# Kernel tuning notes

Hardware: AMD Instinct MI355X
Metric: run time of the kernel (lower is better)

Reference implementation:

```python
import jax, jax.numpy as jnp
import numpy as np

L, D, N = 4096, 1024, 16  # seq_len, d_model, hiddens_per_input


def setup_inputs() -> dict:
    key = jax.random.key(0)
    ks = jax.random.split(key, 9)
    x = jax.random.normal(ks[0], (L, D), dtype=jnp.float32)
    # Delta param (pre-softplus); softplus(Delta) > 0 is the discretization step
    Delta = jax.random.normal(ks[1], (D,), dtype=jnp.float32)
    # A stored as (re, im); default scheme uses A_re = -1 (stable), theta in [0, 2pi)
    A_re = -(0.5 + 0.5 * jax.random.uniform(ks[2], (D, N), dtype=jnp.float32))
    A_im = jax.random.uniform(ks[3], (D, N), dtype=jnp.float32) * 2.0 * jnp.pi
    scale = 1.0 / jnp.sqrt(jnp.float32(D))  # matrix_init: randn / sqrt(shape[0])
    B_re = jax.random.normal(ks[4], (D, N), dtype=jnp.float32) * scale
    B_im = jax.random.normal(ks[5], (D, N), dtype=jnp.float32) * scale
    C_re = jax.random.normal(ks[6], (D, N), dtype=jnp.float32) * scale
    C_im = jax.random.normal(ks[7], (D, N), dtype=jnp.float32) * scale
    D_param = jax.random.normal(ks[8], (D,), dtype=jnp.float32) * scale
    return {"x": x, "Delta": Delta, "A_re": A_re, "A_im": A_im,
            "B_re": B_re, "B_im": B_im, "C_re": C_re, "C_im": C_im,
            "D_param": D_param}


def _binary_operator_diag(q_i, q_j):
    """Associative op for diagonal linear recurrence h_j = A_j h_{j-1} + b_j."""
    A_i, b_i = q_i
    A_j, b_j = q_j
    return (A_j * A_i, A_j * b_i + b_j)


def reference(x, Delta, A_re, A_im, B_re, B_im, C_re, C_im, D_param):
    Bc = B_re + 1j * B_im                      # (D, N) complex
    Cc = C_re + 1j * C_im                      # (D, N) complex
    Ac = A_re + 1j * A_im                      # (D, N) complex
    dt = jax.nn.softplus(Delta)                # (D,)
    # shared_Delta=True branch: Lambda = exp(dt[:, None] * A), repeated over L
    Lam = jnp.exp(dt[:, None] * Ac)            # (D, N) complex
    Lambda_elements = jnp.broadcast_to(Lam[None, :, :], (x.shape[0], *Lam.shape))
    # Bu = einsum('D, D N, L D -> L D N', dt, B, x)
    Bu_elements = jnp.einsum('D,DN,LD->LDN', dt.astype(Bc.dtype), Bc,
                             x.astype(Bc.dtype))
    _, hidden_states = jax.lax.associative_scan(
        _binary_operator_diag, (Lambda_elements, Bu_elements))  # (L, D, N)
    out = jnp.einsum('LDN,DN->LD', hidden_states, Cc) + D_param[None, :] * x
    return out.real
```

## Files before the change

### kernel.cpp

```cpp
#include <hip/hip_runtime.h>
#include <math.h>

constexpr int L   = 4096;
constexpr int D   = 1024;
constexpr int N   = 16;
constexpr int CPB = 2;
constexpr int NB  = D / CPB;
constexpr int NCB = 64;
constexpr int T   = L / NCB;

__device__ __forceinline__ float softplus_f(float v) {
    return fmaxf(v, 0.0f) + log1pf(expf(-fabsf(v)));
}

__device__ __forceinline__ void lam_fast(float ar, float ai, float dt,
                                         float& lr, float& li) {
    float e = __expf(ar * dt);
    float s, c;
    __sincosf(ai * dt, &s, &c);
    lr = e * c;
    li = e * s;
}

__global__ __launch_bounds__(256, 2) void k_fused(
    const float* __restrict__ x,
    const float* __restrict__ Delta,
    const float* __restrict__ A_re, const float* __restrict__ A_im,
    const float* __restrict__ B_re, const float* __restrict__ B_im,
    const float* __restrict__ C_re, const float* __restrict__ C_im,
    const float* __restrict__ Dp,
    float* __restrict__ out)
{
    __shared__ float  xs[T * 128];
    __shared__ float2 sums[NCB * 32];

    const int b  = blockIdx.x;
    const int d0 = (b & 7) * 128 + (b >> 3) * 2;
    const int t  = threadIdx.x;

    {
        const int sct = t & 63;
        const int si  = t >> 6;
        float2 v[16];
        #pragma unroll
        for (int k = 0; k < 16; ++k) {
            int l = sct * T + si * 16 + k;
            v[k] = *(const float2*)(x + (size_t)l * D + d0);
        }
        #pragma unroll
        for (int k = 0; k < 16; ++k) {
            int i = si * 16 + k;
            *(float2*)&xs[i * 128 + sct * 2] = v[k];
        }
    }

    const int h  = t & 1;
    const int dd = (t >> 1) & 1;
    const int ct = t >> 2;
    const int d  = d0 + dd;
    const float dt = softplus_f(Delta[d]);

    float Lr[8], Li[8];
    {
        const int base = d * N + h * 8;
        float4 a0 = *(const float4*)(A_re + base);
        float4 a1 = *(const float4*)(A_re + base + 4);
        float4 m0 = *(const float4*)(A_im + base);
        float4 m1 = *(const float4*)(A_im + base + 4);
        const float ar[8] = {a0.x, a0.y, a0.z, a0.w, a1.x, a1.y, a1.z, a1.w};
        const float ai[8] = {m0.x, m0.y, m0.z, m0.w, m1.x, m1.y, m1.z, m1.w};
        #pragma unroll
        for (int j = 0; j < 8; ++j) lam_fast(ar[j], ai[j], dt, Lr[j], Li[j]);
    }
    __syncthreads();

    float gr[8] = {0, 0, 0, 0, 0, 0, 0, 0}, gi[8] = {0, 0, 0, 0, 0, 0, 0, 0};
    #pragma unroll 8
    for (int i = 0; i < T; ++i) {
        float xv = xs[i * 128 + ct * 2 + dd];
        #pragma unroll
        for (int j = 0; j < 8; ++j) {
            float t2 = fmaf(-Li[j], gi[j], xv);
            float nr = fmaf(Lr[j], gr[j], t2);
            gi[j] = fmaf(Lr[j], gi[j], Li[j] * gr[j]);
            gr[j] = nr;
        }
    }
    {
        float2* sp = &sums[ct * 32 + dd * 16 + h * 8];
        #pragma unroll
        for (int j = 0; j < 8; ++j) sp[j] = make_float2(gr[j], gi[j]);
    }
    __syncthreads();

    if (t < 32) {
        const int dd2 = t >> 4, n2 = t & 15;
        const int d2  = d0 + dd2;
        const float dt2 = softplus_f(Delta[d2]);
        float lr, li;
        lam_fast(A_re[d2 * N + n2], A_im[d2 * N + n2], dt2, lr, li);
        #pragma unroll
        for (int k = 0; k < 6; ++k) {
            float nr = lr * lr - li * li;
            li = 2.0f * lr * li;
            lr = nr;
        }
        float cr = 0.0f, ci = 0.0f;
        #pragma unroll
        for (int c0 = 0; c0 < NCB; c0 += 16) {
            float2 sv[16];
            #pragma unroll
            for (int u = 0; u < 16; ++u) sv[u] = sums[(c0 + u) * 32 + t];
            #pragma unroll
            for (int u = 0; u < 16; ++u) {
                sums[(c0 + u) * 32 + t] = make_float2(cr, ci);
                float nr = fmaf(lr, cr, fmaf(-li, ci, sv[u].x));
                ci = fmaf(lr, ci, fmaf(li, cr, sv[u].y));
                cr = nr;
            }
        }
    }

    float Cr[8], Ci[8];
    {
        const int base = d * N + h * 8;
        float4 b0 = *(const float4*)(B_re + base);
        float4 b1 = *(const float4*)(B_re + base + 4);
        float4 e0 = *(const float4*)(B_im + base);
        float4 e1 = *(const float4*)(B_im + base + 4);
        float4 f0 = *(const float4*)(C_re + base);
        float4 f1 = *(const float4*)(C_re + base + 4);
        float4 g0 = *(const float4*)(C_im + base);
        float4 g1 = *(const float4*)(C_im + base + 4);
        const float br[8] = {b0.x, b0.y, b0.z, b0.w, b1.x, b1.y, b1.z, b1.w};
        const float bi[8] = {e0.x, e0.y, e0.z, e0.w, e1.x, e1.y, e1.z, e1.w};
        const float cr[8] = {f0.x, f0.y, f0.z, f0.w, f1.x, f1.y, f1.z, f1.w};
        const float ci[8] = {g0.x, g0.y, g0.z, g0.w, g1.x, g1.y, g1.z, g1.w};
        #pragma unroll
        for (int j = 0; j < 8; ++j) {
            Cr[j] = dt * (cr[j] * br[j] - ci[j] * bi[j]);
            Ci[j] = dt * (cr[j] * bi[j] + ci[j] * br[j]);
        }
    }
    const float dpv = Dp[d];
    __syncthreads();

    {
        const float2* cp = &sums[ct * 32 + dd * 16 + h * 8];
        #pragma unroll
        for (int j = 0; j < 8; ++j) { gr[j] = cp[j].x; gi[j] = cp[j].y; }
    }
    #pragma unroll 4
    for (int ib = 0; ib < T / 2; ++ib) {
        float keep = 0.0f;
        #pragma unroll
        for (int u = 0; u < 2; ++u) {
            int i = ib * 2 + u;
            float xv = xs[i * 128 + ct * 2 + dd];
            float acc = 0.0f;
            #pragma unroll
            for (int j = 0; j < 8; ++j) {
                float t2 = fmaf(-Li[j], gi[j], xv);
                float nr = fmaf(Lr[j], gr[j], t2);
                gi[j] = fmaf(Lr[j], gi[j], Li[j] * gr[j]);
                gr[j] = nr;
                acc = fmaf(Cr[j], gr[j], acc);
                acc = fmaf(-Ci[j], gi[j], acc);
            }
            acc += __shfl_xor(acc, 1);
            acc = fmaf(dpv, xv, acc);
            keep = (h == u) ? acc : keep;
        }
        out[(size_t)(ct * T + ib * 2 + h) * D + d] = keep;
    }
}

extern "C" void kernel_launch(void* const* d_in, const int* in_sizes, int n_in,
                              void* d_out, int out_size, void* d_ws, size_t ws_size,
                              hipStream_t stream) {
    const float* x     = (const float*)d_in[0];
    const float* Delta = (const float*)d_in[1];
    const float* A_re  = (const float*)d_in[2];
    const float* A_im  = (const float*)d_in[3];
    const float* B_re  = (const float*)d_in[4];
    const float* B_im  = (const float*)d_in[5];
    const float* C_re  = (const float*)d_in[6];
    const float* C_im  = (const float*)d_in[7];
    const float* Dp    = (const float*)d_in[8];
    float* out = (float*)d_out;

    k_fused<<<NB, 256, 0, stream>>>(x, Delta, A_re, A_im, B_re, B_im,
                                    C_re, C_im, Dp, out);
}
```

Baseline: 106.9 us.

## Double chunk count to 128 with 512 threads and pack recurrence into float2 FMAs

```diff
diff --git a/kernel.cpp b/kernel.cpp
--- a/kernel.cpp
+++ b/kernel.cpp
@@ -6,8 +6,11 @@
 constexpr int N   = 16;
 constexpr int CPB = 2;
 constexpr int NB  = D / CPB;
-constexpr int NCB = 64;
+constexpr int NCB = 128;
 constexpr int T   = L / NCB;
+constexpr int NT  = 512;
+
+typedef float v2 __attribute__((ext_vector_type(2)));
 
 __device__ __forceinline__ float softplus_f(float v) {
     return fmaxf(v, 0.0f) + log1pf(expf(-fabsf(v)));
@@ -22,7 +25,11 @@
     li = e * s;
 }
 
-__global__ __launch_bounds__(256, 2) void k_fused(
+__device__ __forceinline__ v2 vfma(v2 a, v2 b, v2 c) {
+    return __builtin_elementwise_fma(a, b, c);
+}
+
+__global__ __launch_bounds__(NT, 4) void k_fused(
     const float* __restrict__ x,
     const float* __restrict__ Delta,
     const float* __restrict__ A_re, const float* __restrict__ A_im,
@@ -31,7 +38,7 @@
     const float* __restrict__ Dp,
     float* __restrict__ out)
 {
-    __shared__ float  xs[T * 128];
+    __shared__ float  xs[T * 256];
     __shared__ float2 sums[NCB * 32];
 
     const int b  = blockIdx.x;
@@ -39,18 +46,18 @@
     const int t  = threadIdx.x;
 
     {
-        const int sct = t & 63;
-        const int si  = t >> 6;
-        float2 v[16];
-        #pragma unroll
-        for (int k = 0; k < 16; ++k) {
-            int l = sct * T + si * 16 + k;
+        const int sct = t & 127;
+        const int si  = t >> 7;
+        float2 v[8];
+        #pragma unroll
+        for (int k = 0; k < 8; ++k) {
+            int l = sct * T + si * 8 + k;
             v[k] = *(const float2*)(x + (size_t)l * D + d0);
         }
         #pragma unroll
-        for (int k = 0; k < 16; ++k) {
-            int i = si * 16 + k;
-            *(float2*)&xs[i * 128 + sct * 2] = v[k];
+        for (int k = 0; k < 8; ++k) {
+            int il = si * 8 + k;
+            *(float2*)&xs[il * 256 + sct * 2] = v[k];
         }
     }
 
@@ -60,7 +67,7 @@
     const int d  = d0 + dd;
     const float dt = softplus_f(Delta[d]);
 
-    float Lr[8], Li[8];
+    v2 LR[4], LI[4];
     {
         const int base = d * N + h * 8;
         float4 a0 = *(const float4*)(A_re + base);
@@ -70,26 +77,37 @@
         const float ar[8] = {a0.x, a0.y, a0.z, a0.w, a1.x, a1.y, a1.z, a1.w};
         const float ai[8] = {m0.x, m0.y, m0.z, m0.w, m1.x, m1.y, m1.z, m1.w};
         #pragma unroll
-        for (int j = 0; j < 8; ++j) lam_fast(ar[j], ai[j], dt, Lr[j], Li[j]);
+        for (int p = 0; p < 4; ++p) {
+            float lr0, li0, lr1, li1;
+            lam_fast(ar[2 * p], ai[2 * p], dt, lr0, li0);
+            lam_fast(ar[2 * p + 1], ai[2 * p + 1], dt, lr1, li1);
+            LR[p] = (v2){lr0, lr1};
+            LI[p] = (v2){li0, li1};
+        }
     }
     __syncthreads();
 
-    float gr[8] = {0, 0, 0, 0, 0, 0, 0, 0}, gi[8] = {0, 0, 0, 0, 0, 0, 0, 0};
-    #pragma unroll 8
+    v2 GR[4] = {(v2)0, (v2)0, (v2)0, (v2)0};
+    v2 GI[4] = {(v2)0, (v2)0, (v2)0, (v2)0};
+    #pragma unroll 4
     for (int i = 0; i < T; ++i) {
-        float xv = xs[i * 128 + ct * 2 + dd];
-        #pragma unroll
-        for (int j = 0; j < 8; ++j) {
-            float t2 = fmaf(-Li[j], gi[j], xv);
-            float nr = fmaf(Lr[j], gr[j], t2);
-            gi[j] = fmaf(Lr[j], gi[j], Li[j] * gr[j]);
-            gr[j] = nr;
+        float xv = xs[i * 256 + ct * 2 + dd];
+        v2 XV = (v2){xv, xv};
+        #pragma unroll
+        for (int p = 0; p < 4; ++p) {
+            v2 t2 = vfma(-LI[p], GI[p], XV);
+            v2 nr = vfma(LR[p], GR[p], t2);
+            GI[p] = vfma(LR[p], GI[p], LI[p] * GR[p]);
+            GR[p] = nr;
         }
     }
     {
         float2* sp = &sums[ct * 32 + dd * 16 + h * 8];
         #pragma unroll
-        for (int j = 0; j < 8; ++j) sp[j] = make_float2(gr[j], gi[j]);
+        for (int p = 0; p < 4; ++p) {
+            sp[2 * p]     = make_float2(GR[p].x, GI[p].x);
+            sp[2 * p + 1] = make_float2(GR[p].y, GI[p].y);
+        }
     }
     __syncthreads();
 
@@ -100,7 +118,7 @@
         float lr, li;
         lam_fast(A_re[d2 * N + n2], A_im[d2 * N + n2], dt2, lr, li);
         #pragma unroll
-        for (int k = 0; k < 6; ++k) {
+        for (int k = 0; k < 5; ++k) {
             float nr = lr * lr - li * li;
             li = 2.0f * lr * li;
             lr = nr;
@@ -121,7 +139,7 @@
         }
     }
 
-    float Cr[8], Ci[8];
+    v2 CR[4], CI[4];
     {
         const int base = d * N + h * 8;
         float4 b0 = *(const float4*)(B_re + base);
@@ -137,9 +155,11 @@
         const float cr[8] = {f0.x, f0.y, f0.z, f0.w, f1.x, f1.y, f1.z, f1.w};
         const float ci[8] = {g0.x, g0.y, g0.z, g0.w, g1.x, g1.y, g1.z, g1.w};
         #pragma unroll
-        for (int j = 0; j < 8; ++j) {
-            Cr[j] = dt * (cr[j] * br[j] - ci[j] * bi[j]);
-            Ci[j] = dt * (cr[j] * bi[j] + ci[j] * br[j]);
+        for (int p = 0; p < 4; ++p) {
+            CR[p] = (v2){dt * (cr[2*p] * br[2*p] - ci[2*p] * bi[2*p]),
+                         dt * (cr[2*p+1] * br[2*p+1] - ci[2*p+1] * bi[2*p+1])};
+            CI[p] = (v2){dt * (cr[2*p] * bi[2*p] + ci[2*p] * br[2*p]),
+                         dt * (cr[2*p+1] * bi[2*p+1] + ci[2*p+1] * br[2*p+1])};
         }
     }
     const float dpv = Dp[d];
@@ -148,7 +168,11 @@
     {
         const float2* cp = &sums[ct * 32 + dd * 16 + h * 8];
         #pragma unroll
-        for (int j = 0; j < 8; ++j) { gr[j] = cp[j].x; gi[j] = cp[j].y; }
+        for (int p = 0; p < 4; ++p) {
+            float2 c0 = cp[2 * p], c1 = cp[2 * p + 1];
+            GR[p] = (v2){c0.x, c1.x};
+            GI[p] = (v2){c0.y, c1.y};
+        }
     }
     #pragma unroll 4
     for (int ib = 0; ib < T / 2; ++ib) {
@@ -156,17 +180,19 @@
         #pragma unroll
         for (int u = 0; u < 2; ++u) {
             int i = ib * 2 + u;
-            float xv = xs[i * 128 + ct * 2 + dd];
-            float acc = 0.0f;
+            float xv = xs[i * 256 + ct * 2 + dd];
+            v2 XV = (v2){xv, xv};
+            v2 ACC = (v2)0;
             #pragma unroll
-            for (int j = 0; j < 8; ++j) {
-                float t2 = fmaf(-Li[j], gi[j], xv);
-                float nr = fmaf(Lr[j], gr[j], t2);
-                gi[j] = fmaf(Lr[j], gi[j], Li[j] * gr[j]);
-                gr[j] = nr;
-                acc = fmaf(Cr[j], gr[j], acc);
-                acc = fmaf(-Ci[j], gi[j], acc);
+            for (int p = 0; p < 4; ++p) {
+                v2 t2 = vfma(-LI[p], GI[p], XV);
+                v2 nr = vfma(LR[p], GR[p], t2);
+                GI[p] = vfma(LR[p], GI[p], LI[p] * GR[p]);
+                GR[p] = nr;
+                ACC = vfma(CR[p], GR[p], ACC);
+                ACC = vfma(-CI[p], GI[p], ACC);
             }
+            float acc = ACC.x + ACC.y;
             acc += __shfl_xor(acc, 1);
             acc = fmaf(dpv, xv, acc);
             keep = (h == u) ? acc : keep;
@@ -189,6 +215,6 @@
     const float* Dp    = (const float*)d_in[8];
     float* out = (float*)d_out;
 
-    k_fused<<<NB, 256, 0, stream>>>(x, Delta, A_re, A_im, B_re, B_im,
-                                    C_re, C_im, Dp, out);
-}
+    k_fused<<<NB, NT, 0, stream>>>(x, Delta, A_re, A_im, B_re, B_im,
+                                   C_re, C_im, Dp, out);
+}
```

Measured after the change: 106.0 us. No clear change (-0.9%).
